# Kernel tuning notes

Measured on AMD Instinct MI355X. Metric: run time of the kernel, lower is better.

Reference implementation:

```python
import jax, jax.numpy as jnp
import numpy as np

T, B, INP = 64, 4, 768
Q = E = 384  # hidden // divisor = 1536 // 4
DFF = 2 * INP


def _binop(ei, ej):
    # masked associative operator for the linear recurrence s_t = f_t*s_{t-1}+c_t
    ui, xi, mi = ei
    uj, xj, mj = ej
    cond = mj > 0
    return (jnp.where(cond, uj, uj * ui),
            jnp.where(cond, xj, uj * xi + xj),
            jnp.where(cond, mj, mi))


def setup_inputs() -> dict:
    key = jax.random.key(0)
    ks = jax.random.split(key, 10)
    n = lambda i, shp: jax.random.normal(ks[i], shp, jnp.float32)
    inp = n(0, (T, B, INP))
    is_first = (jax.random.uniform(ks[1], (T, B, 1)) < 0.05).astype(jnp.float32)
    drops = jnp.ones((T, B, 1), jnp.float32)            # eval-mode dropout mask
    init_inp = jnp.zeros((B, INP), jnp.float32)
    init_state = jnp.zeros((B, Q * E), jnp.float32)
    return {
        'inp': inp, 'is_first': is_first, 'drops': drops,
        'init_inp': init_inp, 'init_state': init_state,
        'mix_mu': jax.random.uniform(ks[2], (INP,), jnp.float32),
        'mix_W': n(3, (INP, Q)) / np.sqrt(INP),
        'layer_W': n(4, (INP, 2 * Q + 2 * E)) / np.sqrt(INP),
        'proj_W': n(5, (E, INP)) / np.sqrt(E),
        'rms_w': jnp.ones((E,), jnp.float32),
        'ln_w': jnp.ones((INP,), jnp.float32),
        'ln_b': jnp.zeros((INP,), jnp.float32),
        'ffn_W1': n(6, (INP, DFF)) / np.sqrt(INP),
        'ffn_W2': n(7, (INP, DFF)) / np.sqrt(INP),
        'ffn_W3': n(8, (DFF, INP)) / np.sqrt(DFF),
    }


def reference(inp, is_first, drops, init_inp, init_state, mix_mu, mix_W,
              layer_W, proj_W, rms_w, ln_w, ln_b, ffn_W1, ffn_W2, ffn_W3):
    Tt, Bb, _ = inp.shape
    Qd, Ed = mix_W.shape[1], proj_W.shape[0]
    init = init_state.reshape(Bb, Qd, Ed)[None]                 # [1,B,Q,E]
    init_masks = jnp.concatenate([jnp.ones_like(is_first[:1]), is_first[1:]], 0)
    lasts = jnp.concatenate([jnp.zeros_like(inp[:1]), inp[:-1]], 0)
    lasts = lasts + init_masks * (init_inp[None] - lasts)
    # components
    mixed = mix_mu * inp + (1.0 - mix_mu) * lasts               # MixingLayer
    forget = jax.nn.sigmoid(mixed @ mix_W)                      # [T,B,Q]
    forget = (forget - 1.0) * drops + 1.0
    parts = (inp @ layer_W) * drops                             # [T,B,2Q+2E]
    qk = jax.nn.elu(parts[..., :2 * Qd]) + 1.0
    query, keyv = qk[..., :Qd], qk[..., Qd:]
    reset, value = parts[..., 2 * Qd:2 * Qd + Ed], parts[..., 2 * Qd + Ed:]
    value = jax.nn.sigmoid(reset) * value
    cand = keyv[..., :, None] * value[..., None, :]             # [T,B,Q,E]
    forget_b = jnp.broadcast_to(forget[..., None], cand.shape)
    cands = cand + init_masks[..., None] * forget_b * init
    masks = jnp.broadcast_to(is_first[..., None], cand.shape)
    # masked log-depth parallel scan of s_t = f_t*s_{t-1} + c_t
    states = jax.lax.associative_scan(_binop, (forget_b, cands, masks), axis=0)[1]
    out = jnp.einsum('tbq,tbqe->tbe', query, states)            # query @ state
    out = out * jax.lax.rsqrt(jnp.mean(out * out, -1, keepdims=True) + 1e-6) * rms_w
    out = out @ proj_W                                          # [T,B,INP]
    # RNNCell: residual + LayerNorm + gated FFN (SwiGLU-style GatingLayer)
    h = inp + out
    mu = jnp.mean(h, -1, keepdims=True)
    var = jnp.var(h, -1, keepdims=True)
    h = (h - mu) * jax.lax.rsqrt(var + 1e-5) * ln_w + ln_b
    return (jax.nn.silu(h @ ffn_W1) * (h @ ffn_W2)) @ ffn_W3
```

## Files before the change

### kernel.cpp

```cpp
#include <hip/hip_runtime.h>
#include <hip/hip_bf16.h>

#define T_DIM 64
#define B_DIM 4
#define INP_D 768
#define Q_D   384
#define E_D   384
#define DFF_D 1536
#define NTOK  256

typedef short bf16x8 __attribute__((ext_vector_type(8)));
typedef float f32x4  __attribute__((ext_vector_type(4)));

__device__ __forceinline__ float sigf(float x)  { return 1.0f / (1.0f + __expf(-x)); }
__device__ __forceinline__ float elu1f(float x) { return x > 0.0f ? x + 1.0f : __expf(x); }

__device__ __forceinline__ short f2b(float x) {
  union { __hip_bfloat16 b; short s; } u;
  u.b = __float2bfloat16(x);
  return u.s;
}
__device__ __forceinline__ bf16x8 cvt8(float4 a, float4 b) {
  bf16x8 r;
  r[0] = f2b(a.x); r[1] = f2b(a.y); r[2] = f2b(a.z); r[3] = f2b(a.w);
  r[4] = f2b(b.x); r[5] = f2b(b.y); r[6] = f2b(b.z); r[7] = f2b(b.w);
  return r;
}

#define WS_FORGET 0
#define WS_QUERY  98304
#define WS_KEYV   196608
#define WS_VALUE  294912
#define WS_PATT   393216
#define WS_ATTN   1179648
#define WS_HPRE   1277952
#define WS_H      1474560
#define WS_G      1671168
#define WS_BF     2064384
#define PK_MIX   0
#define PK_LAYER 294912
#define PK_PROJ  1474560
#define PK_W1    1769472
#define PK_W2    2949120
#define PK_W3    4128768

__global__ __launch_bounds__(256) void k_conv(const float* __restrict__ mixW,
                                              const float* __restrict__ layerW,
                                              const float* __restrict__ projW,
                                              const float* __restrict__ W1,
                                              const float* __restrict__ W2,
                                              const float* __restrict__ W3,
                                              short* __restrict__ wsb) {
  const int blk = blockIdx.x;
  const float* src; short* dst; int N, kb, nb64;
  if (blk < 144)        { src = mixW;   dst = wsb + PK_MIX;   N = 384;  int r = blk;        kb = r / 6;  nb64 = r % 6; }
  else if (blk < 720)   { src = layerW; dst = wsb + PK_LAYER; N = 1536; int r = blk - 144;  kb = r / 24; nb64 = r % 24; }
  else if (blk < 864)   { src = projW;  dst = wsb + PK_PROJ;  N = 768;  int r = blk - 720;  kb = r / 12; nb64 = r % 12; }
  else if (blk < 1440)  { src = W1;     dst = wsb + PK_W1;    N = 1536; int r = blk - 864;  kb = r / 24; nb64 = r % 24; }
  else if (blk < 2016)  { src = W2;     dst = wsb + PK_W2;    N = 1536; int r = blk - 1440; kb = r / 24; nb64 = r % 24; }
  else                  { src = W3;     dst = wsb + PK_W3;    N = 768;  int r = blk - 2016; kb = r / 12; nb64 = r % 12; }

  __shared__ float lds[32][68];
  const int tid = threadIdx.x;
  {
    const int r = tid >> 3, c8 = (tid & 7) * 8;
    const float* p = &src[(size_t)(kb * 32 + r) * N + nb64 * 64 + c8];
    *(float4*)&lds[r][c8]     = *(const float4*)p;
    *(float4*)&lds[r][c8 + 4] = *(const float4*)(p + 4);
  }
  __syncthreads();
  {
    const int nb = tid >> 6, lane = tid & 63, g = lane >> 4, c = lane & 15;
    unsigned int w[4];
#pragma unroll
    for (int jj = 0; jj < 4; ++jj) {
      unsigned short lo = (unsigned short)f2b(lds[g * 8 + jj * 2][nb * 16 + c]);
      unsigned short hi = (unsigned short)f2b(lds[g * 8 + jj * 2 + 1][nb * 16 + c]);
      w[jj] = (unsigned int)lo | ((unsigned int)hi << 16);
    }
    const int N16 = N >> 4;
    size_t o = ((size_t)kb * N16 + (nb64 * 4 + nb)) * 512 + lane * 8;
    uint4 pk; pk.x = w[0]; pk.y = w[1]; pk.z = w[2]; pk.w = w[3];
    *(uint4*)&dst[o] = pk;
  }
}

template<int KSTEPS, int SUBT, bool DUAL, class ALoad>
__device__ __forceinline__ void mm_core(ALoad loadA,
                                        const short* __restrict__ B1, int bn1, int N16a,
                                        const short* __restrict__ B2, int bn2, int N16b,
                                        int lane, f32x4* acc1, f32x4* acc2) {
  bf16x8 a_c = loadA(0);
  bf16x8 b1c[SUBT], b2c[SUBT];
#pragma unroll
  for (int s = 0; s < SUBT; ++s)
    b1c[s] = *(const bf16x8*)&B1[((size_t)(bn1 + s)) * 512 + lane * 8];
  if constexpr (DUAL) {
#pragma unroll
    for (int s = 0; s < SUBT; ++s)
      b2c[s] = *(const bf16x8*)&B2[((size_t)(bn2 + s)) * 512 + lane * 8];
  }
#pragma unroll 2
  for (int kb = 0; kb < KSTEPS; ++kb) {
    bf16x8 a_n = a_c;
    bf16x8 b1n[SUBT], b2n[SUBT];
    if (kb + 1 < KSTEPS) {
      a_n = loadA(kb + 1);
#pragma unroll
      for (int s = 0; s < SUBT; ++s)
        b1n[s] = *(const bf16x8*)&B1[((size_t)(kb + 1) * N16a + bn1 + s) * 512 + lane * 8];
      if constexpr (DUAL) {
#pragma unroll
        for (int s = 0; s < SUBT; ++s)
          b2n[s] = *(const bf16x8*)&B2[((size_t)(kb + 1) * N16b + bn2 + s) * 512 + lane * 8];
      }
    }
#pragma unroll
    for (int s = 0; s < SUBT; ++s)
      acc1[s] = __builtin_amdgcn_mfma_f32_16x16x32_bf16(a_c, b1c[s], acc1[s], 0, 0, 0);
    if constexpr (DUAL) {
#pragma unroll
      for (int s = 0; s < SUBT; ++s)
        acc2[s] = __builtin_amdgcn_mfma_f32_16x16x32_bf16(a_c, b2c[s], acc2[s], 0, 0, 0);
    }
    a_c = a_n;
#pragma unroll
    for (int s = 0; s < SUBT; ++s) b1c[s] = b1n[s];
    if constexpr (DUAL) {
#pragma unroll
      for (int s = 0; s < SUBT; ++s) b2c[s] = b2n[s];
    }
  }
}

#define WAVE_SETUP  const int tid = threadIdx.x, w = tid >> 6, l = tid & 63; \
                    const int m0 = blockIdx.x * 64; \
                    const int rowA = m0 + w * 16 + (l & 15); \
                    const int kg = (l >> 4) * 8; (void)kg;

__global__ __launch_bounds__(256) void k_qkvfg(const float* __restrict__ inp,
                                               const float* __restrict__ is_first,
                                               const float* __restrict__ init_inp,
                                               const float* __restrict__ mu,
                                               const short* __restrict__ Mixp,
                                               const short* __restrict__ Lp,
                                               const float* __restrict__ drops,
                                               float* __restrict__ forget,
                                               float* __restrict__ query,
                                               float* __restrict__ keyv,
                                               float* __restrict__ value) {
  WAVE_SETUP
  const int y = blockIdx.y;
  if (y < 12) {
    const int n0 = y * 32, bn = y * 2;
    const int tt = rowA >> 2, bb = rowA & 3;
    const float fr = (tt == 0) ? 1.0f : is_first[rowA];
    const float* lastp = (fr > 0.5f) ? &init_inp[bb * INP_D] : &inp[(size_t)(rowA - 4) * INP_D];
    const float* inpp  = &inp[(size_t)rowA * INP_D];
    auto loadA = [&](int kb) -> bf16x8 {
      const int k = kb * 32 + kg;
      float4 x0 = *(const float4*)&inpp[k],  x1 = *(const float4*)&inpp[k + 4];
      float4 l0 = *(const float4*)&lastp[k], l1 = *(const float4*)&lastp[k + 4];
      float4 m0v = *(const float4*)&mu[k],   m1v = *(const float4*)&mu[k + 4];
      float4 r0, r1;
      r0.x = m0v.x * x0.x + (1.0f - m0v.x) * l0.x;
      r0.y = m0v.y * x0.y + (1.0f - m0v.y) * l0.y;
      r0.z = m0v.z * x0.z + (1.0f - m0v.z) * l0.z;
      r0.w = m0v.w * x0.w + (1.0f - m0v.w) * l0.w;
      r1.x = m1v.x * x1.x + (1.0f - m1v.x) * l1.x;
      r1.y = m1v.y * x1.y + (1.0f - m1v.y) * l1.y;
      r1.z = m1v.z * x1.z + (1.0f - m1v.z) * l1.z;
      r1.w = m1v.w * x1.w + (1.0f - m1v.w) * l1.w;
      return cvt8(r0, r1);
    };
    f32x4 acc[2] = {(f32x4){0.f,0.f,0.f,0.f}, (f32x4){0.f,0.f,0.f,0.f}};
    mm_core<24, 2, false>(loadA, Mixp, bn, 24, nullptr, 0, 0, l, acc, nullptr);
#pragma unroll
    for (int i = 0; i < 4; ++i) {
      const int row = m0 + w * 16 + ((l >> 4) << 2) + i;
      const float d = drops[row];
#pragma unroll
      for (int s = 0; s < 2; ++s) {
        const int col = n0 + s * 16 + (l & 15);
        forget[(size_t)row * Q_D + col] = (sigf(acc[s][i]) - 1.0f) * d + 1.0f;
      }
    }
    return;
  }
  const float* Ap = &inp[(size_t)rowA * INP_D];
  auto loadA = [&](int kb) -> bf16x8 {
    const int k = kb * 32 + kg;
    return cvt8(*(const float4*)&Ap[k], *(const float4*)&Ap[k + 4]);
  };
  if (y < 36) {
    const bool isq = (y < 24);
    const int yy = isq ? y - 12 : y - 24;
    float* dst = isq ? query : keyv;
    const int bn = (isq ? 0 : 24) + yy * 2;
    f32x4 acc[2] = {(f32x4){0.f,0.f,0.f,0.f}, (f32x4){0.f,0.f,0.f,0.f}};
    mm_core<24, 2, false>(loadA, Lp, bn, 96, nullptr, 0, 0, l, acc, nullptr);
#pragma unroll
    for (int i = 0; i < 4; ++i) {
      const int row = m0 + w * 16 + ((l >> 4) << 2) + i;
      const float d = drops[row];
#pragma unroll
      for (int s = 0; s < 2; ++s) {
        const int col = yy * 32 + s * 16 + (l & 15);
        dst[(size_t)row * Q_D + col] = elu1f(acc[s][i] * d);
      }
    }
  } else {
    const int q = y - 36;
    const int bn_r = 48 + q * 2, bn_v = 72 + q * 2;
    f32x4 a1[2] = {(f32x4){0.f,0.f,0.f,0.f}, (f32x4){0.f,0.f,0.f,0.f}};
    f32x4 a2[2] = {(f32x4){0.f,0.f,0.f,0.f}, (f32x4){0.f,0.f,0.f,0.f}};
    mm_core<24, 2, true>(loadA, Lp, bn_r, 96, Lp, bn_v, 96, l, a1, a2);
#pragma unroll
    for (int i = 0; i < 4; ++i) {
      const int row = m0 + w * 16 + ((l >> 4) << 2) + i;
      const float d = drops[row];
#pragma unroll
      for (int s = 0; s < 2; ++s) {
        const int col = q * 32 + s * 16 + (l & 15);
        value[(size_t)row * E_D + col] = sigf(a1[s][i] * d) * (a2[s][i] * d);
      }
    }
  }
}

__global__ __launch_bounds__(256) void k_proj(const float* __restrict__ attn,
                                              const short* __restrict__ Bp,
                                              const float* __restrict__ inp,
                                              float* __restrict__ hpre) {
  WAVE_SETUP
  const int n0 = blockIdx.y * 32, bn = blockIdx.y * 2;
  const float* Ap = &attn[(size_t)rowA * E_D];
  auto loadA = [&](int kb) -> bf16x8 {
    const int k = kb * 32 + kg;
    return cvt8(*(const float4*)&Ap[k], *(const float4*)&Ap[k + 4]);
  };
  f32x4 acc[2] = {(f32x4){0.f,0.f,0.f,0.f}, (f32x4){0.f,0.f,0.f,0.f}};
  mm_core<12, 2, false>(loadA, Bp, bn, 48, nullptr, 0, 0, l, acc, nullptr);
#pragma unroll
  for (int i = 0; i < 4; ++i) {
    const int row = m0 + w * 16 + ((l >> 4) << 2) + i;
#pragma unroll
    for (int s = 0; s < 2; ++s) {
      const int col = n0 + s * 16 + (l & 15);
      hpre[(size_t)row * INP_D + col] = acc[s][i] + inp[(size_t)row * INP_D + col];
    }
  }
}

__global__ __launch_bounds__(256) void k_ffn(const float* __restrict__ h,
                                             const short* __restrict__ W1p,
                                             const short* __restrict__ W2p,
                                             float* __restrict__ g) {
  WAVE_SETUP
  const int n0 = blockIdx.y * 32, bn = blockIdx.y * 2;
  const float* Ap = &h[(size_t)rowA * INP_D];
  auto loadA = [&](int kb) -> bf16x8 {
    const int k = kb * 32 + kg;
    return cvt8(*(const float4*)&Ap[k], *(const float4*)&Ap[k + 4]);
  };
  f32x4 a1[2] = {(f32x4){0.f,0.f,0.f,0.f}, (f32x4){0.f,0.f,0.f,0.f}};
  f32x4 a2[2] = {(f32x4){0.f,0.f,0.f,0.f}, (f32x4){0.f,0.f,0.f,0.f}};
  mm_core<24, 2, true>(loadA, W1p, bn, 96, W2p, bn, 96, l, a1, a2);
#pragma unroll
  for (int i = 0; i < 4; ++i) {
    const int row = m0 + w * 16 + ((l >> 4) << 2) + i;
#pragma unroll
    for (int s = 0; s < 2; ++s) {
      const int col = n0 + s * 16 + (l & 15);
      const float v1 = a1[s][i], v2 = a2[s][i];
      g[(size_t)row * DFF_D + col] = v1 * sigf(v1) * v2;
    }
  }
}

__global__ __launch_bounds__(256) void k_out(const float* __restrict__ g,
                                             const short* __restrict__ Bp,
                                             float* __restrict__ out) {
  WAVE_SETUP
  const int n0 = blockIdx.y * 32, bn = blockIdx.y * 2;
  const float* Ap = &g[(size_t)rowA * DFF_D];
  auto loadA = [&](int kb) -> bf16x8 {
    const int k = kb * 32 + kg;
    return cvt8(*(const float4*)&Ap[k], *(const float4*)&Ap[k + 4]);
  };
  f32x4 acc[2] = {(f32x4){0.f,0.f,0.f,0.f}, (f32x4){0.f,0.f,0.f,0.f}};
  mm_core<48, 2, false>(loadA, Bp, bn, 48, nullptr, 0, 0, l, acc, nullptr);
#pragma unroll
  for (int i = 0; i < 4; ++i) {
    const int row = m0 + w * 16 + ((l >> 4) << 2) + i;
#pragma unroll
    for (int s = 0; s < 2; ++s) {
      const int col = n0 + s * 16 + (l & 15);
      out[(size_t)row * INP_D + col] = acc[s][i];
    }
  }
}

__global__ __launch_bounds__(256) void k_scan(const float* __restrict__ forget,
                                              const float* __restrict__ query,
                                              const float* __restrict__ keyv,
                                              const float* __restrict__ value,
                                              const float* __restrict__ is_first,
                                              const float* __restrict__ init_state,
                                              float* __restrict__ patt) {
  __shared__ float stg[144];
  __shared__ float pacc[256];
  const int tid = threadIdx.x;
  const int e  = blockIdx.x * 64 + (tid & 63);
  const int qg = tid >> 6;
  const int qc = blockIdx.y;
  const int b  = blockIdx.z;
  const int q0 = qc * 48 + qg * 12;

  float s[12], ini[12];
#pragma unroll
  for (int j = 0; j < 12; ++j) {
    ini[j] = init_state[((size_t)b * Q_D + q0 + j) * E_D + e];
    s[j]   = ini[j];
  }

  float stage_r = 0.0f, v_r, if_r;
  {
    const int tok = b;
    if (tid < 144) {
      const int which = tid / 48, o = tid % 48;
      const float* src = which == 0 ? forget : (which == 1 ? keyv : query);
      stage_r = src[(size_t)tok * Q_D + qc * 48 + o];
    }
    v_r  = value[(size_t)tok * E_D + e];
    if_r = 0.0f;
  }

  for (int t = 0; t < T_DIM; ++t) {
    const int tok = t * B_DIM + b;
    if (tid < 144) stg[tid] = stage_r;
    const float v  = v_r;
    const float ff = if_r;
    __syncthreads();
    if (t + 1 < T_DIM) {
      const int tok1 = tok + B_DIM;
      if (tid < 144) {
        const int which = tid / 48, o = tid % 48;
        const float* src = which == 0 ? forget : (which == 1 ? keyv : query);
        stage_r = src[(size_t)tok1 * Q_D + qc * 48 + o];
      }
      v_r  = value[(size_t)tok1 * E_D + e];
      if_r = is_first[tok1];
    }
    if (ff > 0.5f) {
#pragma unroll
      for (int j = 0; j < 12; ++j) s[j] = ini[j];
    }
    const float4* f4 = (const float4*)&stg[qg * 12];
    const float4* k4 = (const float4*)&stg[48 + qg * 12];
    const float4* q4 = (const float4*)&stg[96 + qg * 12];
    float p = 0.0f;
#pragma unroll
    for (int jj = 0; jj < 3; ++jj) {
      const float4 fv = f4[jj], kv = k4[jj], qv = q4[jj];
#pragma unroll
      for (int j2 = 0; j2 < 4; ++j2) {
        const int sj = jj * 4 + j2;
        s[sj] = fmaf((&fv.x)[j2], s[sj], (&kv.x)[j2] * v);
        p     = fmaf((&qv.x)[j2], s[sj], p);
      }
    }
    pacc[tid] = p;
    __syncthreads();
    if (tid < 64) {
      float r = pacc[tid] + pacc[tid + 64] + pacc[tid + 128] + pacc[tid + 192];
      patt[((size_t)qc * NTOK + tok) * E_D + blockIdx.x * 64 + tid] = r;
    }
    __syncthreads();
  }
}

__global__ __launch_bounds__(128) void ep_rms(const float* __restrict__ patt,
                                              const float* __restrict__ rms_w,
                                              float* __restrict__ attn) {
  const int tok = blockIdx.x, tid = threadIdx.x;
  float x[3], ss = 0.0f;
#pragma unroll
  for (int i = 0; i < 3; ++i) {
    const int e = i * 128 + tid;
    float a = 0.0f;
#pragma unroll
    for (int qc = 0; qc < 8; ++qc) a += patt[((size_t)qc * NTOK + tok) * E_D + e];
    x[i] = a;
    ss = fmaf(a, a, ss);
  }
#pragma unroll
  for (int off = 32; off; off >>= 1) ss += __shfl_down(ss, off, 64);
  __shared__ float r[2];
  const int wid = tid >> 6, lane = tid & 63;
  if (lane == 0) r[wid] = ss;
  __syncthreads();
  ss = r[0] + r[1];
  const float sc = rsqrtf(ss * (1.0f / E_D) + 1e-6f);
#pragma unroll
  for (int i = 0; i < 3; ++i) {
    const int e = i * 128 + tid;
    attn[(size_t)tok * E_D + e] = x[i] * sc * rms_w[e];
  }
}

__global__ __launch_bounds__(256) void ep_ln(const float* __restrict__ hpre,
                                             const float* __restrict__ ln_w,
                                             const float* __restrict__ ln_b,
                                             float* __restrict__ h) {
  const int tok = blockIdx.x, tid = threadIdx.x;
  float x[3], s1 = 0.0f, s2 = 0.0f;
#pragma unroll
  for (int i = 0; i < 3; ++i) {
    x[i] = hpre[(size_t)tok * INP_D + i * 256 + tid];
    s1 += x[i];
    s2 = fmaf(x[i], x[i], s2);
  }
#pragma unroll
  for (int off = 32; off; off >>= 1) {
    s1 += __shfl_down(s1, off, 64);
    s2 += __shfl_down(s2, off, 64);
  }
  __shared__ float r1[4], r2[4];
  const int wid = tid >> 6, lane = tid & 63;
  if (lane == 0) { r1[wid] = s1; r2[wid] = s2; }
  __syncthreads();
  s1 = r1[0] + r1[1] + r1[2] + r1[3];
  s2 = r2[0] + r2[1] + r2[2] + r2[3];
  const float mean = s1 * (1.0f / INP_D);
  const float var  = s2 * (1.0f / INP_D) - mean * mean;
  const float sc   = rsqrtf(var + 1e-5f);
#pragma unroll
  for (int i = 0; i < 3; ++i) {
    const int c = i * 256 + tid;
    h[(size_t)tok * INP_D + c] = (x[i] - mean) * sc * ln_w[c] + ln_b[c];
  }
}

extern "C" void kernel_launch(void* const* d_in, const int* in_sizes, int n_in,
                              void* d_out, int out_size, void* d_ws, size_t ws_size,
                              hipStream_t stream) {
  (void)in_sizes; (void)n_in; (void)out_size; (void)ws_size;
  const float* inp        = (const float*)d_in[0];
  const float* is_first   = (const float*)d_in[1];
  const float* drops      = (const float*)d_in[2];
  const float* init_inp   = (const float*)d_in[3];
  const float* init_state = (const float*)d_in[4];
  const float* mix_mu     = (const float*)d_in[5];
  const float* mix_W      = (const float*)d_in[6];
  const float* layer_W    = (const float*)d_in[7];
  const float* proj_W     = (const float*)d_in[8];
  const float* rms_w      = (const float*)d_in[9];
  const float* ln_w       = (const float*)d_in[10];
  const float* ln_b       = (const float*)d_in[11];
  const float* W1         = (const float*)d_in[12];
  const float* W2         = (const float*)d_in[13];
  const float* W3         = (const float*)d_in[14];
  float* out = (float*)d_out;
  float* ws  = (float*)d_ws;
  short* wsb = (short*)(ws + WS_BF);

  float* forget = ws + WS_FORGET;
  float* query  = ws + WS_QUERY;
  float* keyv   = ws + WS_KEYV;
  float* value  = ws + WS_VALUE;
  float* patt   = ws + WS_PATT;
  float* attn   = ws + WS_ATTN;
  float* hpre   = ws + WS_HPRE;
  float* h      = ws + WS_H;
  float* g      = ws + WS_G;

  k_conv<<<2592, 256, 0, stream>>>(mix_W, layer_W, proj_W, W1, W2, W3, wsb);
  k_qkvfg<<<dim3(4, 48), 256, 0, stream>>>(inp, is_first, init_inp, mix_mu,
                                           wsb + PK_MIX, wsb + PK_LAYER, drops,
                                           forget, query, keyv, value);
  k_scan<<<dim3(6, 8, 4), 256, 0, stream>>>(forget, query, keyv, value,
                                            is_first, init_state, patt);
  ep_rms<<<NTOK, 128, 0, stream>>>(patt, rms_w, attn);
  k_proj<<<dim3(4, 24), 256, 0, stream>>>(attn, wsb + PK_PROJ, inp, hpre);
  ep_ln<<<NTOK, 256, 0, stream>>>(hpre, ln_w, ln_b, h);
  k_ffn<<<dim3(4, 48), 256, 0, stream>>>(h, wsb + PK_W1, wsb + PK_W2, g);
  k_out<<<dim3(4, 24), 256, 0, stream>>>(g, wsb + PK_W3, out);
}
```

Baseline: 194.4 us.

## Store GEMM activations as bf16 and double-buffer scan staging

Intermediate activations (attn, LN output, FFN gate output) are now written directly as bf16 by their producer epilogues. The input and the mixed input are converted to bf16 inside the weight-conversion kernel, so GEMM A-operand loads read bf16 with no per-k-step fp32 conversion. This halves activation traffic and drops repeated conversion work across the N-tiles. The scan kernel double-buffers its shared staging and pacc arrays, which removes one barrier per timestep at the cost of extra shared memory.

```diff
diff --git a/kernel.cpp b/kernel.cpp
--- a/kernel.cpp
+++ b/kernel.cpp
@@ -32,19 +32,25 @@
 #define WS_KEYV   196608
 #define WS_VALUE  294912
 #define WS_PATT   393216
-#define WS_ATTN   1179648
-#define WS_HPRE   1277952
-#define WS_H      1474560
-#define WS_G      1671168
-#define WS_BF     2064384
-#define PK_MIX   0
-#define PK_LAYER 294912
-#define PK_PROJ  1474560
-#define PK_W1    1769472
-#define PK_W2    2949120
-#define PK_W3    4128768
-
-__global__ __launch_bounds__(256) void k_conv(const float* __restrict__ mixW,
+#define WS_HPRE   1179648
+#define WS_BF     1376256
+#define PB_INP   0
+#define PB_MIXED 196608
+#define PB_ATTN  393216
+#define PB_H     491520
+#define PB_G     688128
+#define PK_MIX   1081344
+#define PK_LAYER 1376256
+#define PK_PROJ  2555904
+#define PK_W1    2850816
+#define PK_W2    4030464
+#define PK_W3    5210112
+
+__global__ __launch_bounds__(256) void k_conv(const float* __restrict__ inp,
+                                              const float* __restrict__ is_first,
+                                              const float* __restrict__ init_inp,
+                                              const float* __restrict__ mu,
+                                              const float* __restrict__ mixW,
                                               const float* __restrict__ layerW,
                                               const float* __restrict__ projW,
                                               const float* __restrict__ W1,
@@ -52,6 +58,34 @@
                                               const float* __restrict__ W3,
                                               short* __restrict__ wsb) {
   const int blk = blockIdx.x;
+  const int tid = threadIdx.x;
+  if (blk >= 2592) {
+    if (blk < 2688) {
+      const int idx = (blk - 2592) * 2048 + tid * 8;
+      float4 a = *(const float4*)&inp[idx], b = *(const float4*)&inp[idx + 4];
+      *(bf16x8*)&wsb[PB_INP + idx] = cvt8(a, b);
+    } else {
+      const int idx = (blk - 2688) * 2048 + tid * 8;
+      const int c = idx % INP_D, tok = idx / INP_D;
+      const int t = tok >> 2, b = tok & 3;
+      const float fr = (t == 0) ? 1.0f : is_first[tok];
+      const float* lastp = (fr > 0.5f) ? &init_inp[b * INP_D + c] : &inp[idx - 4 * INP_D];
+      float4 x0 = *(const float4*)&inp[idx], x1 = *(const float4*)&inp[idx + 4];
+      float4 l0 = *(const float4*)&lastp[0], l1 = *(const float4*)&lastp[4];
+      float4 m0 = *(const float4*)&mu[c],    m1 = *(const float4*)&mu[c + 4];
+      float4 r0, r1;
+      r0.x = m0.x * x0.x + (1.0f - m0.x) * l0.x;
+      r0.y = m0.y * x0.y + (1.0f - m0.y) * l0.y;
+      r0.z = m0.z * x0.z + (1.0f - m0.z) * l0.z;
+      r0.w = m0.w * x0.w + (1.0f - m0.w) * l0.w;
+      r1.x = m1.x * x1.x + (1.0f - m1.x) * l1.x;
+      r1.y = m1.y * x1.y + (1.0f - m1.y) * l1.y;
+      r1.z = m1.z * x1.z + (1.0f - m1.z) * l1.z;
+      r1.w = m1.w * x1.w + (1.0f - m1.w) * l1.w;
+      *(bf16x8*)&wsb[PB_MIXED + idx] = cvt8(r0, r1);
+    }
+    return;
+  }
   const float* src; short* dst; int N, kb, nb64;
   if (blk < 144)        { src = mixW;   dst = wsb + PK_MIX;   N = 384;  int r = blk;        kb = r / 6;  nb64 = r % 6; }
   else if (blk < 720)   { src = layerW; dst = wsb + PK_LAYER; N = 1536; int r = blk - 144;  kb = r / 24; nb64 = r % 24; }
@@ -61,7 +95,6 @@
   else                  { src = W3;     dst = wsb + PK_W3;    N = 768;  int r = blk - 2016; kb = r / 12; nb64 = r % 12; }
 
   __shared__ float lds[32][68];
-  const int tid = threadIdx.x;
   {
     const int r = tid >> 3, c8 = (tid & 7) * 8;
     const float* p = &src[(size_t)(kb * 32 + r) * N + nb64 * 64 + c8];
@@ -85,12 +118,12 @@
   }
 }
 
-template<int KSTEPS, int SUBT, bool DUAL, class ALoad>
-__device__ __forceinline__ void mm_core(ALoad loadA,
+template<int KSTEPS, int SUBT, bool DUAL, int ASTRIDE>
+__device__ __forceinline__ void mm_core(const short* __restrict__ Arow, int kg,
                                         const short* __restrict__ B1, int bn1, int N16a,
                                         const short* __restrict__ B2, int bn2, int N16b,
                                         int lane, f32x4* acc1, f32x4* acc2) {
-  bf16x8 a_c = loadA(0);
+  bf16x8 a_c = *(const bf16x8*)&Arow[kg];
   bf16x8 b1c[SUBT], b2c[SUBT];
 #pragma unroll
   for (int s = 0; s < SUBT; ++s)
@@ -105,7 +138,7 @@
     bf16x8 a_n = a_c;
     bf16x8 b1n[SUBT], b2n[SUBT];
     if (kb + 1 < KSTEPS) {
-      a_n = loadA(kb + 1);
+      a_n = *(const bf16x8*)&Arow[(kb + 1) * 32 + kg];
 #pragma unroll
       for (int s = 0; s < SUBT; ++s)
         b1n[s] = *(const bf16x8*)&B1[((size_t)(kb + 1) * N16a + bn1 + s) * 512 + lane * 8];
@@ -138,10 +171,8 @@
                     const int rowA = m0 + w * 16 + (l & 15); \
                     const int kg = (l >> 4) * 8; (void)kg;
 
-__global__ __launch_bounds__(256) void k_qkvfg(const float* __restrict__ inp,
-                                               const float* __restrict__ is_first,
-                                               const float* __restrict__ init_inp,
-                                               const float* __restrict__ mu,
+__global__ __launch_bounds__(256) void k_qkvfg(const short* __restrict__ inp_bf,
+                                               const short* __restrict__ mixed_bf,
                                                const short* __restrict__ Mixp,
                                                const short* __restrict__ Lp,
                                                const float* __restrict__ drops,
@@ -153,28 +184,9 @@
   const int y = blockIdx.y;
   if (y < 12) {
     const int n0 = y * 32, bn = y * 2;
-    const int tt = rowA >> 2, bb = rowA & 3;
-    const float fr = (tt == 0) ? 1.0f : is_first[rowA];
-    const float* lastp = (fr > 0.5f) ? &init_inp[bb * INP_D] : &inp[(size_t)(rowA - 4) * INP_D];
-    const float* inpp  = &inp[(size_t)rowA * INP_D];
-    auto loadA = [&](int kb) -> bf16x8 {
-      const int k = kb * 32 + kg;
-      float4 x0 = *(const float4*)&inpp[k],  x1 = *(const float4*)&inpp[k + 4];
-      float4 l0 = *(const float4*)&lastp[k], l1 = *(const float4*)&lastp[k + 4];
-      float4 m0v = *(const float4*)&mu[k],   m1v = *(const float4*)&mu[k + 4];
-      float4 r0, r1;
-      r0.x = m0v.x * x0.x + (1.0f - m0v.x) * l0.x;
-      r0.y = m0v.y * x0.y + (1.0f - m0v.y) * l0.y;
-      r0.z = m0v.z * x0.z + (1.0f - m0v.z) * l0.z;
-      r0.w = m0v.w * x0.w + (1.0f - m0v.w) * l0.w;
-      r1.x = m1v.x * x1.x + (1.0f - m1v.x) * l1.x;
-      r1.y = m1v.y * x1.y + (1.0f - m1v.y) * l1.y;
-      r1.z = m1v.z * x1.z + (1.0f - m1v.z) * l1.z;
-      r1.w = m1v.w * x1.w + (1.0f - m1v.w) * l1.w;
-      return cvt8(r0, r1);
-    };
+    const short* Arow = &mixed_bf[(size_t)rowA * INP_D];
     f32x4 acc[2] = {(f32x4){0.f,0.f,0.f,0.f}, (f32x4){0.f,0.f,0.f,0.f}};
-    mm_core<24, 2, false>(loadA, Mixp, bn, 24, nullptr, 0, 0, l, acc, nullptr);
+    mm_core<24, 2, false, INP_D>(Arow, kg, Mixp, bn, 24, nullptr, 0, 0, l, acc, nullptr);
 #pragma unroll
     for (int i = 0; i < 4; ++i) {
       const int row = m0 + w * 16 + ((l >> 4) << 2) + i;
@@ -187,18 +199,14 @@
     }
     return;
   }
-  const float* Ap = &inp[(size_t)rowA * INP_D];
-  auto loadA = [&](int kb) -> bf16x8 {
-    const int k = kb * 32 + kg;
-    return cvt8(*(const float4*)&Ap[k], *(const float4*)&Ap[k + 4]);
-  };
+  const short* Arow = &inp_bf[(size_t)rowA * INP_D];
   if (y < 36) {
     const bool isq = (y < 24);
     const int yy = isq ? y - 12 : y - 24;
     float* dst = isq ? query : keyv;
     const int bn = (isq ? 0 : 24) + yy * 2;
     f32x4 acc[2] = {(f32x4){0.f,0.f,0.f,0.f}, (f32x4){0.f,0.f,0.f,0.f}};
-    mm_core<24, 2, false>(loadA, Lp, bn, 96, nullptr, 0, 0, l, acc, nullptr);
+    mm_core<24, 2, false, INP_D>(Arow, kg, Lp, bn, 96, nullptr, 0, 0, l, acc, nullptr);
 #pragma unroll
     for (int i = 0; i < 4; ++i) {
       const int row = m0 + w * 16 + ((l >> 4) << 2) + i;
@@ -214,7 +222,7 @@
     const int bn_r = 48 + q * 2, bn_v = 72 + q * 2;
     f32x4 a1[2] = {(f32x4){0.f,0.f,0.f,0.f}, (f32x4){0.f,0.f,0.f,0.f}};
     f32x4 a2[2] = {(f32x4){0.f,0.f,0.f,0.f}, (f32x4){0.f,0.f,0.f,0.f}};
-    mm_core<24, 2, true>(loadA, Lp, bn_r, 96, Lp, bn_v, 96, l, a1, a2);
+    mm_core<24, 2, true, INP_D>(Arow, kg, Lp, bn_r, 96, Lp, bn_v, 96, l, a1, a2);
 #pragma unroll
     for (int i = 0; i < 4; ++i) {
       const int row = m0 + w * 16 + ((l >> 4) << 2) + i;
@@ -228,19 +236,15 @@
   }
 }
 
-__global__ __launch_bounds__(256) void k_proj(const float* __restrict__ attn,
+__global__ __launch_bounds__(256) void k_proj(const short* __restrict__ attn_bf,
                                               const short* __restrict__ Bp,
                                               const float* __restrict__ inp,
                                               float* __restrict__ hpre) {
   WAVE_SETUP
   const int n0 = blockIdx.y * 32, bn = blockIdx.y * 2;
-  const float* Ap = &attn[(size_t)rowA * E_D];
-  auto loadA = [&](int kb) -> bf16x8 {
-    const int k = kb * 32 + kg;
-    return cvt8(*(const float4*)&Ap[k], *(const float4*)&Ap[k + 4]);
-  };
+  const short* Arow = &attn_bf[(size_t)rowA * E_D];
   f32x4 acc[2] = {(f32x4){0.f,0.f,0.f,0.f}, (f32x4){0.f,0.f,0.f,0.f}};
-  mm_core<12, 2, false>(loadA, Bp, bn, 48, nullptr, 0, 0, l, acc, nullptr);
+  mm_core<12, 2, false, E_D>(Arow, kg, Bp, bn, 48, nullptr, 0, 0, l, acc, nullptr);
 #pragma unroll
   for (int i = 0; i < 4; ++i) {
     const int row = m0 + w * 16 + ((l >> 4) << 2) + i;
@@ -252,20 +256,16 @@
   }
 }
 
-__global__ __launch_bounds__(256) void k_ffn(const float* __restrict__ h,
+__global__ __launch_bounds__(256) void k_ffn(const short* __restrict__ h_bf,
                                              const short* __restrict__ W1p,
                                              const short* __restrict__ W2p,
-                                             float* __restrict__ g) {
+                                             short* __restrict__ g_bf) {
   WAVE_SETUP
   const int n0 = blockIdx.y * 32, bn = blockIdx.y * 2;
-  const float* Ap = &h[(size_t)rowA * INP_D];
-  auto loadA = [&](int kb) -> bf16x8 {
-    const int k = kb * 32 + kg;
-    return cvt8(*(const float4*)&Ap[k], *(const float4*)&Ap[k + 4]);
-  };
+  const short* Arow = &h_bf[(size_t)rowA * INP_D];
   f32x4 a1[2] = {(f32x4){0.f,0.f,0.f,0.f}, (f32x4){0.f,0.f,0.f,0.f}};
   f32x4 a2[2] = {(f32x4){0.f,0.f,0.f,0.f}, (f32x4){0.f,0.f,0.f,0.f}};
-  mm_core<24, 2, true>(loadA, W1p, bn, 96, W2p, bn, 96, l, a1, a2);
+  mm_core<24, 2, true, INP_D>(Arow, kg, W1p, bn, 96, W2p, bn, 96, l, a1, a2);
 #pragma unroll
   for (int i = 0; i < 4; ++i) {
     const int row = m0 + w * 16 + ((l >> 4) << 2) + i;
@@ -273,23 +273,19 @@
     for (int s = 0; s < 2; ++s) {
       const int col = n0 + s * 16 + (l & 15);
       const float v1 = a1[s][i], v2 = a2[s][i];
-      g[(size_t)row * DFF_D + col] = v1 * sigf(v1) * v2;
-    }
-  }
-}
-
-__global__ __launch_bounds__(256) void k_out(const float* __restrict__ g,
+      g_bf[(size_t)row * DFF_D + col] = f2b(v1 * sigf(v1) * v2);
+    }
+  }
+}
+
+__global__ __launch_bounds__(256) void k_out(const short* __restrict__ g_bf,
                                              const short* __restrict__ Bp,
                                              float* __restrict__ out) {
   WAVE_SETUP
   const int n0 = blockIdx.y * 32, bn = blockIdx.y * 2;
-  const float* Ap = &g[(size_t)rowA * DFF_D];
-  auto loadA = [&](int kb) -> bf16x8 {
-    const int k = kb * 32 + kg;
-    return cvt8(*(const float4*)&Ap[k], *(const float4*)&Ap[k + 4]);
-  };
+  const short* Arow = &g_bf[(size_t)rowA * DFF_D];
   f32x4 acc[2] = {(f32x4){0.f,0.f,0.f,0.f}, (f32x4){0.f,0.f,0.f,0.f}};
-  mm_core<48, 2, false>(loadA, Bp, bn, 48, nullptr, 0, 0, l, acc, nullptr);
+  mm_core<48, 2, false, DFF_D>(Arow, kg, Bp, bn, 48, nullptr, 0, 0, l, acc, nullptr);
 #pragma unroll
   for (int i = 0; i < 4; ++i) {
     const int row = m0 + w * 16 + ((l >> 4) << 2) + i;
@@ -308,8 +304,8 @@
                                               const float* __restrict__ is_first,
                                               const float* __restrict__ init_state,
                                               float* __restrict__ patt) {
-  __shared__ float stg[144];
-  __shared__ float pacc[256];
+  __shared__ float stg[2][144];
+  __shared__ float pacc[2][256];
   const int tid = threadIdx.x;
   const int e  = blockIdx.x * 64 + (tid & 63);
   const int qg = tid >> 6;
@@ -324,41 +320,35 @@
     s[j]   = ini[j];
   }
 
-  float stage_r = 0.0f, v_r, if_r;
-  {
-    const int tok = b;
-    if (tid < 144) {
-      const int which = tid / 48, o = tid % 48;
-      const float* src = which == 0 ? forget : (which == 1 ? keyv : query);
-      stage_r = src[(size_t)tok * Q_D + qc * 48 + o];
-    }
-    v_r  = value[(size_t)tok * E_D + e];
-    if_r = 0.0f;
-  }
+  auto stageld = [&](int tok) -> float {
+    const int which = tid / 48, o = tid % 48;
+    const float* src = which == 0 ? forget : (which == 1 ? keyv : query);
+    return src[(size_t)tok * Q_D + qc * 48 + o];
+  };
+
+  float v_c, if_c;
+  if (tid < 144) stg[0][tid] = stageld(b);
+  v_c  = value[(size_t)b * E_D + e];
+  if_c = 0.0f;
+  __syncthreads();
 
   for (int t = 0; t < T_DIM; ++t) {
     const int tok = t * B_DIM + b;
-    if (tid < 144) stg[tid] = stage_r;
-    const float v  = v_r;
-    const float ff = if_r;
-    __syncthreads();
+    const int cur = t & 1;
+    float stage_n = 0.0f, v_n = 0.0f, if_n = 0.0f;
     if (t + 1 < T_DIM) {
       const int tok1 = tok + B_DIM;
-      if (tid < 144) {
-        const int which = tid / 48, o = tid % 48;
-        const float* src = which == 0 ? forget : (which == 1 ? keyv : query);
-        stage_r = src[(size_t)tok1 * Q_D + qc * 48 + o];
-      }
-      v_r  = value[(size_t)tok1 * E_D + e];
-      if_r = is_first[tok1];
-    }
-    if (ff > 0.5f) {
+      if (tid < 144) stage_n = stageld(tok1);
+      v_n  = value[(size_t)tok1 * E_D + e];
+      if_n = is_first[tok1];
+    }
+    if (if_c > 0.5f) {
 #pragma unroll
       for (int j = 0; j < 12; ++j) s[j] = ini[j];
     }
-    const float4* f4 = (const float4*)&stg[qg * 12];
-    const float4* k4 = (const float4*)&stg[48 + qg * 12];
-    const float4* q4 = (const float4*)&stg[96 + qg * 12];
+    const float4* f4 = (const float4*)&stg[cur][qg * 12];
+    const float4* k4 = (const float4*)&stg[cur][48 + qg * 12];
+    const float4* q4 = (const float4*)&stg[cur][96 + qg * 12];
     float p = 0.0f;
 #pragma unroll
     for (int jj = 0; jj < 3; ++jj) {
@@ -366,23 +356,25 @@
 #pragma unroll
       for (int j2 = 0; j2 < 4; ++j2) {
         const int sj = jj * 4 + j2;
-        s[sj] = fmaf((&fv.x)[j2], s[sj], (&kv.x)[j2] * v);
+        s[sj] = fmaf((&fv.x)[j2], s[sj], (&kv.x)[j2] * v_c);
         p     = fmaf((&qv.x)[j2], s[sj], p);
       }
     }
-    pacc[tid] = p;
+    pacc[cur][tid] = p;
+    if (t + 1 < T_DIM && tid < 144) stg[cur ^ 1][tid] = stage_n;
     __syncthreads();
     if (tid < 64) {
-      float r = pacc[tid] + pacc[tid + 64] + pacc[tid + 128] + pacc[tid + 192];
+      float r = pacc[cur][tid] + pacc[cur][tid + 64] + pacc[cur][tid + 128] + pacc[cur][tid + 192];
       patt[((size_t)qc * NTOK + tok) * E_D + blockIdx.x * 64 + tid] = r;
     }
-    __syncthreads();
+    v_c  = v_n;
+    if_c = if_n;
   }
 }
 
 __global__ __launch_bounds__(128) void ep_rms(const float* __restrict__ patt,
                                               const float* __restrict__ rms_w,
-                                              float* __restrict__ attn) {
+                                              short* __restrict__ attn_bf) {
   const int tok = blockIdx.x, tid = threadIdx.x;
   float x[3], ss = 0.0f;
 #pragma unroll
@@ -405,14 +397,14 @@
 #pragma unroll
   for (int i = 0; i < 3; ++i) {
     const int e = i * 128 + tid;
-    attn[(size_t)tok * E_D + e] = x[i] * sc * rms_w[e];
+    attn_bf[(size_t)tok * E_D + e] = f2b(x[i] * sc * rms_w[e]);
   }
 }
 
 __global__ __launch_bounds__(256) void ep_ln(const float* __restrict__ hpre,
                                              const float* __restrict__ ln_w,
                                              const float* __restrict__ ln_b,
-                                             float* __restrict__ h) {
+                                             short* __restrict__ h_bf) {
   const int tok = blockIdx.x, tid = threadIdx.x;
   float x[3], s1 = 0.0f, s2 = 0.0f;
 #pragma unroll
@@ -438,7 +430,7 @@
 #pragma unroll
   for (int i = 0; i < 3; ++i) {
     const int c = i * 256 + tid;
-    h[(size_t)tok * INP_D + c] = (x[i] - mean) * sc * ln_w[c] + ln_b[c];
+    h_bf[(size_t)tok * INP_D + c] = f2b((x[i] - mean) * sc * ln_w[c] + ln_b[c]);
   }
 }
 
@@ -470,20 +462,18 @@
   float* keyv   = ws + WS_KEYV;
   float* value  = ws + WS_VALUE;
   float* patt   = ws + WS_PATT;
-  float* attn   = ws + WS_ATTN;
   float* hpre   = ws + WS_HPRE;
-  float* h      = ws + WS_H;
-  float* g      = ws + WS_G;
-
-  k_conv<<<2592, 256, 0, stream>>>(mix_W, layer_W, proj_W, W1, W2, W3, wsb);
-  k_qkvfg<<<dim3(4, 48), 256, 0, stream>>>(inp, is_first, init_inp, mix_mu,
+
+  k_conv<<<2784, 256, 0, stream>>>(inp, is_first, init_inp, mix_mu,
+                                   mix_W, layer_W, proj_W, W1, W2, W3, wsb);
+  k_qkvfg<<<dim3(4, 48), 256, 0, stream>>>(wsb + PB_INP, wsb + PB_MIXED,
                                            wsb + PK_MIX, wsb + PK_LAYER, drops,
                                            forget, query, keyv, value);
   k_scan<<<dim3(6, 8, 4), 256, 0, stream>>>(forget, query, keyv, value,
                                             is_first, init_state, patt);
-  ep_rms<<<NTOK, 128, 0, stream>>>(patt, rms_w, attn);
-  k_proj<<<dim3(4, 24), 256, 0, stream>>>(attn, wsb + PK_PROJ, inp, hpre);
-  ep_ln<<<NTOK, 256, 0, stream>>>(hpre, ln_w, ln_b, h);
-  k_ffn<<<dim3(4, 48), 256, 0, stream>>>(h, wsb + PK_W1, wsb + PK_W2, g);
-  k_out<<<dim3(4, 24), 256, 0, stream>>>(g, wsb + PK_W3, out);
-}
+  ep_rms<<<NTOK, 128, 0, stream>>>(patt, rms_w, wsb + PB_ATTN);
+  k_proj<<<dim3(4, 24), 256, 0, stream>>>(wsb + PB_ATTN, wsb + PK_PROJ, inp, hpre);
+  ep_ln<<<NTOK, 256, 0, stream>>>(hpre, ln_w, ln_b, wsb + PB_H);
+  k_ffn<<<dim3(4, 48), 256, 0, stream>>>(wsb + PB_H, wsb + PK_W1, wsb + PK_W2, wsb + PB_G);
+  k_out<<<dim3(4, 24), 256, 0, stream>>>(wsb + PB_G, wsb + PK_W3, out);
+}
```

Result: slower. 198.7 us (+2.2%).
